# Performance work log

Hardware: AMD Instinct MI355X
Metric: run time of the kernel (lower is better)

The kernel has to match this reference:

```python
import jax, jax.numpy as jnp
import numpy as np

NUM_RELATIONS = 8
DROP_P = 0.2


def rgcn_layer(x, W, root, b, edge_index, edge_type, num_relations):
    # x: [N,F], W: [R,F,O], root: [F,O], b: [O]
    # edge_index: [2,E] (row 0 = source, row 1 = target), edge_type: [E]
    src, dst = edge_index[0], edge_index[1]
    N = x.shape[0]
    O = W.shape[2]
    # Transform all nodes under every relation once: [R,N,O]
    transformed = jnp.einsum('nf,rfo->rno', x, W)
    msg = transformed[edge_type, src]  # [E,O] gather per edge
    # mean aggregation per relation: per-(relation,target) in-degree
    deg = jnp.zeros((num_relations, N), x.dtype).at[edge_type, dst].add(1.0)
    coef = (1.0 / jnp.clip(deg, 1.0))[edge_type, dst]  # [E]
    agg = jnp.zeros((N, O), x.dtype).at[dst].add(msg * coef[:, None])
    return agg + x @ root + b


def setup_inputs() -> dict:
    key = jax.random.key(0)
    ks = jax.random.split(key, 10)
    N, E, F, H, O, R = 50000, 400000, 128, 128, 64, NUM_RELATIONS
    x = jax.random.normal(ks[0], (N, F), jnp.float32)
    edge_index = jax.random.randint(ks[1], (2, E), 0, N, jnp.int64)
    edge_type = jax.random.randint(ks[2], (E,), 0, R, jnp.int64)
    s = 1.0 / np.sqrt(F)
    W1 = jax.random.normal(ks[3], (R, F, H), jnp.float32) * s
    root1 = jax.random.normal(ks[4], (F, H), jnp.float32) * s
    b1 = jnp.zeros((H,), jnp.float32)
    sh = 1.0 / np.sqrt(H)
    W2 = jax.random.normal(ks[5], (R, H, O), jnp.float32) * sh
    root2 = jax.random.normal(ks[6], (H, O), jnp.float32) * sh
    b2 = jnp.zeros((O,), jnp.float32)
    # inverted dropout mask (training mode, p=0.2), precomputed for determinism
    keep = jax.random.bernoulli(ks[7], 1.0 - DROP_P, (N, H))
    drop_mask = keep.astype(jnp.float32) / (1.0 - DROP_P)
    return {"x": x, "edge_index": edge_index, "edge_type": edge_type,
            "W1": W1, "root1": root1, "b1": b1,
            "W2": W2, "root2": root2, "b2": b2, "drop_mask": drop_mask}


def reference(x, edge_index, edge_type, W1, root1, b1, W2, root2, b2, drop_mask):
    h = rgcn_layer(x, W1, root1, b1, edge_index, edge_type, NUM_RELATIONS)
    h = jax.nn.relu(h) * drop_mask  # fused relu + dropout
    out = rgcn_layer(h, W2, root2, b2, edge_index, edge_type, NUM_RELATIONS)
    return out
```

## Files before the change

### kernel.cpp

```cpp
#include <hip/hip_runtime.h>
#include <hip/hip_bf16.h>
#include <stdint.h>

typedef __attribute__((ext_vector_type(8))) short bf16x8;
typedef __attribute__((ext_vector_type(4))) float f32x4;

__device__ __forceinline__ unsigned f2bf(float f){
  unsigned u = __builtin_bit_cast(unsigned, f);
  return (u + 0x7FFFu + ((u >> 16) & 1u)) >> 16;
}
__device__ __forceinline__ float bf2f(unsigned s){
  unsigned u = s << 16; return __builtin_bit_cast(float, u);
}
__device__ __forceinline__ void add8(float* a, uint4 g){
  a[0] += bf2f(g.x & 0xFFFFu); a[1] += bf2f(g.x >> 16);
  a[2] += bf2f(g.y & 0xFFFFu); a[3] += bf2f(g.y >> 16);
  a[4] += bf2f(g.z & 0xFFFFu); a[5] += bf2f(g.z >> 16);
  a[6] += bf2f(g.w & 0xFFFFu); a[7] += bf2f(g.w >> 16);
}

__global__ void k_combo(const float* __restrict__ x,
                        const float* __restrict__ W1, const float* __restrict__ r1,
                        const float* __restrict__ W2, const float* __restrict__ r2,
                        const int* __restrict__ ei, const int* __restrict__ et,
                        short* __restrict__ Wt1, short* __restrict__ Wt2,
                        uint2* __restrict__ xb, int* __restrict__ degr,
                        int N, int E, int WB, int XB){
  int b = blockIdx.x, tid = threadIdx.x;
  if (b < WB){
    int t = b * 256 + tid;
    if (t < 128 * 1152){
      int o = t / 1152, ka = t - o * 1152, ph = ka >> 7, k = ka & 127;
      int kk = k >> 5, q = (k >> 3) & 3, j = k & 7;
      float v = (ph < 8) ? W1[(ph * 128 + k) * 128 + o] : r1[k * 128 + o];
      Wt1[(((ph * 4 + kk) * 4 + q) * 128 + o) * 8 + j] = (short)f2bf(v);
    } else if (t < 128 * 1152 + 64 * 1152){
      int t2 = t - 128 * 1152;
      int o = t2 / 1152, ka = t2 - o * 1152, ph = ka >> 7, k = ka & 127;
      int kk = k >> 5, q = (k >> 3) & 3, j = k & 7;
      float v = (ph < 8) ? W2[(ph * 128 + k) * 64 + o] : r2[k * 64 + o];
      Wt2[(((ph * 4 + kk) * 4 + q) * 64 + o) * 8 + j] = (short)f2bf(v);
    }
  } else if (b < WB + XB){
    int t = (b - WB) * 256 + tid;
    if (t < N * 32){
      float4 v = reinterpret_cast<const float4*>(x)[t];
      uint2 o;
      o.x = f2bf(v.x) | (f2bf(v.y) << 16);
      o.y = f2bf(v.z) | (f2bf(v.w) << 16);
      xb[t] = o;
    }
  } else {
    int e = (b - WB - XB) * 256 + tid;
    if (e < E){
      unsigned dst = (unsigned)ei[E + e];
      int rel = et[e] & 7;
      if (dst < (unsigned)N) atomicAdd(&degr[rel * N + dst], 1);
    }
  }
}

__global__ void k_scan(const int* __restrict__ cnt, int* __restrict__ gcnt,
                       int* __restrict__ offs, unsigned* __restrict__ pmeta, int M){
  __shared__ int s[256];
  __shared__ int sbase;
  int i = blockIdx.x * 256 + threadIdx.x;
  int v = (i < M) ? cnt[i] : 0;
  s[threadIdx.x] = v; __syncthreads();
  for (int d = 1; d < 256; d <<= 1){
    int t = (threadIdx.x >= d) ? s[threadIdx.x - d] : 0;
    __syncthreads();
    s[threadIdx.x] += t;
    __syncthreads();
  }
  if (threadIdx.x == 255) sbase = atomicAdd(gcnt, s[255]);
  __syncthreads();
  if (i < M){
    int off = sbase + s[threadIdx.x] - v;
    offs[i] = off;
    int c = v; if (c > 4095) c = 4095;
    pmeta[i] = (unsigned)off | ((unsigned)c << 20);
  }
}

__global__ void k_fill(const int* __restrict__ ei, const int* __restrict__ et,
                       const int* __restrict__ offs, int* __restrict__ fill,
                       unsigned short* __restrict__ idx, int E, int N){
  int e = blockIdx.x * 256 + threadIdx.x;
  if (e >= E) return;
  unsigned src = (unsigned)ei[e];
  unsigned dst = (unsigned)ei[E + e];
  int rel = et[e] & 7;
  if (dst < (unsigned)N){
    int key = rel * N + (int)dst;
    int p = atomicAdd(&fill[key], 1);
    idx[offs[key] + p] = (unsigned short)src;
  }
}

template<int NF, int MODE>
__global__ __launch_bounds__(256, 4)
void k_fused(const short* __restrict__ feat, const unsigned* __restrict__ pmeta,
             const unsigned short* __restrict__ idx2, const short* __restrict__ Wt,
             const float* __restrict__ bias, const float* __restrict__ mask,
             void* __restrict__ outp, int N){
  constexpr int BN = NF * 16;
  constexpr int NPW = NF / 4;
  __shared__ char sA[9 * 16 * 256];
  int tid = threadIdx.x, lane = tid & 63, wave = tid >> 6;
  int row0 = blockIdx.x * 16;

  {
    int r = tid >> 4, l = tid & 15;
    int dstj = row0 + r;
    bool vd = dstj < N;
    int dsafe = vd ? dstj : 0;
    unsigned m[8];
    #pragma unroll
    for (int ph = 0; ph < 8; ph++) m[ph] = vd ? pmeta[ph * N + dstj] : 0u;
    int s0[8], s1[8];
    #pragma unroll
    for (int ph = 0; ph < 8; ph++){
      int cnt = (int)(m[ph] >> 20), base = (int)(m[ph] & 0xFFFFFu);
      s0[ph] = (cnt > 0) ? (int)idx2[base] : 0;
      s1[ph] = (cnt > 1) ? (int)idx2[base + 1] : 0;
    }
    uint4 g0[8], g1[8], gr;
    #pragma unroll
    for (int ph = 0; ph < 8; ph++)
      g0[ph] = *reinterpret_cast<const uint4*>(feat + (size_t)s0[ph] * 128 + l * 8);
    #pragma unroll
    for (int ph = 0; ph < 8; ph++)
      g1[ph] = *reinterpret_cast<const uint4*>(feat + (size_t)s1[ph] * 128 + l * 8);
    gr = *reinterpret_cast<const uint4*>(feat + (size_t)dsafe * 128 + l * 8);

    int swz = (l ^ (r & 7)) << 4;
    #pragma unroll
    for (int ph = 0; ph < 8; ph++){
      int cnt = (int)(m[ph] >> 20), base = (int)(m[ph] & 0xFFFFFu);
      uint4 ov = {0u, 0u, 0u, 0u};
      if (cnt > 0){
        float a[8];
        a[0]=bf2f(g0[ph].x&0xFFFFu); a[1]=bf2f(g0[ph].x>>16);
        a[2]=bf2f(g0[ph].y&0xFFFFu); a[3]=bf2f(g0[ph].y>>16);
        a[4]=bf2f(g0[ph].z&0xFFFFu); a[5]=bf2f(g0[ph].z>>16);
        a[6]=bf2f(g0[ph].w&0xFFFFu); a[7]=bf2f(g0[ph].w>>16);
        if (cnt > 1) add8(a, g1[ph]);
        for (int i = 2; i < cnt; i++){
          int s = (int)idx2[base + i];
          uint4 gi = *reinterpret_cast<const uint4*>(feat + (size_t)s * 128 + l * 8);
          add8(a, gi);
        }
        float inv = 1.0f / (float)cnt;
        ov.x = f2bf(a[0]*inv) | (f2bf(a[1]*inv) << 16);
        ov.y = f2bf(a[2]*inv) | (f2bf(a[3]*inv) << 16);
        ov.z = f2bf(a[4]*inv) | (f2bf(a[5]*inv) << 16);
        ov.w = f2bf(a[6]*inv) | (f2bf(a[7]*inv) << 16);
      }
      *reinterpret_cast<uint4*>(sA + ph * 4096 + r * 256 + swz) = ov;
    }
    *reinterpret_cast<uint4*>(sA + 8 * 4096 + r * 256 + swz) = gr;
  }

  int r16 = lane & 15, q = lane >> 4;
  int obase = wave * NPW * 16 + r16;
  bf16x8 bb[2][4][NPW];
  #pragma unroll
  for (int kk = 0; kk < 4; kk++)
    #pragma unroll
    for (int nn = 0; nn < NPW; nn++)
      bb[0][kk][nn] = *reinterpret_cast<const bf16x8*>(
          Wt + ((size_t)(kk * 4 + q) * BN + obase + nn * 16) * 8);

  __syncthreads();

  f32x4 acc[NPW];
  f32x4 z = {0.f, 0.f, 0.f, 0.f};
  #pragma unroll
  for (int nn = 0; nn < NPW; nn++) acc[nn] = z;

  #pragma unroll
  for (int ph = 0; ph < 9; ph++){
    if (ph < 8){
      #pragma unroll
      for (int kk = 0; kk < 4; kk++)
        #pragma unroll
        for (int nn = 0; nn < NPW; nn++)
          bb[(ph + 1) & 1][kk][nn] = *reinterpret_cast<const bf16x8*>(
              Wt + ((size_t)(((ph + 1) * 4 + kk) * 4 + q) * BN + obase + nn * 16) * 8);
    }
    #pragma unroll
    for (int kk = 0; kk < 4; kk++){
      int ch = ((kk * 4 + q) ^ (r16 & 7)) << 4;
      bf16x8 av = *reinterpret_cast<const bf16x8*>(sA + ph * 4096 + r16 * 256 + ch);
      #pragma unroll
      for (int nn = 0; nn < NPW; nn++)
        acc[nn] = __builtin_amdgcn_mfma_f32_16x16x32_bf16(av, bb[ph & 1][kk][nn],
                                                          acc[nn], 0, 0, 0);
    }
  }

  #pragma unroll
  for (int nn = 0; nn < NPW; nn++){
    int col = obase + nn * 16;
    float bv = bias[col];
    #pragma unroll
    for (int j = 0; j < 4; j++){
      int row = row0 + (q << 2) + j;
      if (row < N){
        float v = acc[nn][j] + bv;
        if (MODE == 1){
          v = fmaxf(v, 0.f) * mask[(size_t)row * 128 + col];
          reinterpret_cast<short*>(outp)[(size_t)row * 128 + col] = (short)f2bf(v);
        } else {
          reinterpret_cast<float*>(outp)[(size_t)row * BN + col] = v;
        }
      }
    }
  }
}

extern "C" void kernel_launch(void* const* d_in, const int* in_sizes, int n_in,
                              void* d_out, int out_size, void* d_ws, size_t ws_size,
                              hipStream_t stream){
  const float* x    = (const float*)d_in[0];
  const int*   ei   = (const int*)d_in[1];
  const int*   et   = (const int*)d_in[2];
  const float* W1   = (const float*)d_in[3];
  const float* r1   = (const float*)d_in[4];
  const float* b1   = (const float*)d_in[5];
  const float* W2   = (const float*)d_in[6];
  const float* r2   = (const float*)d_in[7];
  const float* b2   = (const float*)d_in[8];
  const float* mask = (const float*)d_in[9];
  int N = in_sizes[0] / 128;
  int E = in_sizes[2];
  int M8 = 8 * N;

  char* ws = (char*)d_ws;
  short*    xb    = (short*)(ws + 0);
  short*    hb    = (short*)(ws + 12800000);
  short*    Wt1   = (short*)(ws + 25600000);
  short*    Wt2   = (short*)(ws + 25894912);
  int*      degr  = (int*)(ws + 26042368);
  int*      fill  = (int*)(ws + 27642368);
  int*      gcnt  = (int*)(ws + 29242368);
  int*      offs2 = (int*)(ws + 29242432);
  unsigned* pmeta = (unsigned*)(ws + 30842432);
  unsigned short* idx2 = (unsigned short*)(ws + 32442432);
  if (ws_size < (size_t)32442432 + (size_t)E * 2 + 64) return;

  hipMemsetAsync(degr, 0, (size_t)M8 * 8 + 64, stream);

  int WB = (128*1152 + 64*1152 + 255) / 256;
  int XB = (N * 32 + 255) / 256;
  int EB = (E + 255) / 256;
  int NB = (M8 + 255) / 256;
  k_combo<<<WB + XB + EB, 256, 0, stream>>>(x, W1, r1, W2, r2, ei, et,
                                            Wt1, Wt2, (uint2*)xb, degr, N, E, WB, XB);
  k_scan<<<NB, 256, 0, stream>>>(degr, gcnt, offs2, pmeta, M8);
  k_fill<<<EB, 256, 0, stream>>>(ei, et, offs2, fill, idx2, E, N);

  int G = (N + 15) / 16;
  k_fused<8, 1><<<G, 256, 0, stream>>>(xb, pmeta, idx2, Wt1, b1, mask, hb, N);
  k_fused<4, 2><<<G, 256, 0, stream>>>(hb, pmeta, idx2, Wt2, b2, nullptr, d_out, N);
}
```

Before: 281.3 us.

## Stage first gathered neighbor rows directly into LDS and stream weights per MFMA

The first neighbor row per relation is now loaded with global_load_lds straight into shared memory, with zero-padded sentinel rows so empty relations need no branching. Nodes with more than one neighbor accumulate and rewrite their LDS slot. The self-row is held in registers instead of a ninth LDS phase. Weight fragments are read from global memory right before each MFMA instead of being double-buffered in registers, which cuts register pressure but exposes load latency. The workspace layout gains padding so the sentinel rows can be zeroed.

After: 284.6 us. No clear change (+1.2%).

```diff
diff --git a/kernel.cpp b/kernel.cpp
--- a/kernel.cpp
+++ b/kernel.cpp
@@ -17,6 +17,10 @@
   a[2] += bf2f(g.y & 0xFFFFu); a[3] += bf2f(g.y >> 16);
   a[4] += bf2f(g.z & 0xFFFFu); a[5] += bf2f(g.z >> 16);
   a[6] += bf2f(g.w & 0xFFFFu); a[7] += bf2f(g.w >> 16);
+}
+__device__ __forceinline__ void stage16(const void* g, void* l){
+  __builtin_amdgcn_global_load_lds((const __attribute__((address_space(1))) void*)g,
+                                   (__attribute__((address_space(3))) void*)l, 16, 0, 0);
 }
 
 __global__ void k_combo(const float* __restrict__ x,
@@ -106,97 +110,96 @@
              void* __restrict__ outp, int N){
   constexpr int BN = NF * 16;
   constexpr int NPW = NF / 4;
-  __shared__ char sA[9 * 16 * 256];
+  __shared__ char sA[8 * 16 * 256];
   int tid = threadIdx.x, lane = tid & 63, wave = tid >> 6;
   int row0 = blockIdx.x * 16;
-
-  {
-    int r = tid >> 4, l = tid & 15;
-    int dstj = row0 + r;
-    bool vd = dstj < N;
-    int dsafe = vd ? dstj : 0;
-    unsigned m[8];
-    #pragma unroll
-    for (int ph = 0; ph < 8; ph++) m[ph] = vd ? pmeta[ph * N + dstj] : 0u;
-    int s0[8], s1[8];
-    #pragma unroll
-    for (int ph = 0; ph < 8; ph++){
-      int cnt = (int)(m[ph] >> 20), base = (int)(m[ph] & 0xFFFFFu);
-      s0[ph] = (cnt > 0) ? (int)idx2[base] : 0;
-      s1[ph] = (cnt > 1) ? (int)idx2[base + 1] : 0;
-    }
-    uint4 g0[8], g1[8], gr;
-    #pragma unroll
-    for (int ph = 0; ph < 8; ph++)
-      g0[ph] = *reinterpret_cast<const uint4*>(feat + (size_t)s0[ph] * 128 + l * 8);
-    #pragma unroll
-    for (int ph = 0; ph < 8; ph++)
-      g1[ph] = *reinterpret_cast<const uint4*>(feat + (size_t)s1[ph] * 128 + l * 8);
-    gr = *reinterpret_cast<const uint4*>(feat + (size_t)dsafe * 128 + l * 8);
-
-    int swz = (l ^ (r & 7)) << 4;
-    #pragma unroll
-    for (int ph = 0; ph < 8; ph++){
-      int cnt = (int)(m[ph] >> 20), base = (int)(m[ph] & 0xFFFFFu);
-      uint4 ov = {0u, 0u, 0u, 0u};
-      if (cnt > 0){
-        float a[8];
-        a[0]=bf2f(g0[ph].x&0xFFFFu); a[1]=bf2f(g0[ph].x>>16);
-        a[2]=bf2f(g0[ph].y&0xFFFFu); a[3]=bf2f(g0[ph].y>>16);
-        a[4]=bf2f(g0[ph].z&0xFFFFu); a[5]=bf2f(g0[ph].z>>16);
-        a[6]=bf2f(g0[ph].w&0xFFFFu); a[7]=bf2f(g0[ph].w>>16);
-        if (cnt > 1) add8(a, g1[ph]);
-        for (int i = 2; i < cnt; i++){
-          int s = (int)idx2[base + i];
-          uint4 gi = *reinterpret_cast<const uint4*>(feat + (size_t)s * 128 + l * 8);
-          add8(a, gi);
-        }
-        float inv = 1.0f / (float)cnt;
-        ov.x = f2bf(a[0]*inv) | (f2bf(a[1]*inv) << 16);
-        ov.y = f2bf(a[2]*inv) | (f2bf(a[3]*inv) << 16);
-        ov.z = f2bf(a[4]*inv) | (f2bf(a[5]*inv) << 16);
-        ov.w = f2bf(a[6]*inv) | (f2bf(a[7]*inv) << 16);
-      }
-      *reinterpret_cast<uint4*>(sA + ph * 4096 + r * 256 + swz) = ov;
-    }
-    *reinterpret_cast<uint4*>(sA + 8 * 4096 + r * 256 + swz) = gr;
+  int r = tid >> 4, l = tid & 15;
+  int dstj = row0 + r;
+  bool vd = dstj < N;
+  int c = l ^ (r & 7);
+
+  unsigned m[8];
+  #pragma unroll
+  for (int ph = 0; ph < 8; ph++) m[ph] = vd ? pmeta[ph * N + dstj] : 0u;
+  int s0[8];
+  #pragma unroll
+  for (int ph = 0; ph < 8; ph++){
+    int cnt = (int)(m[ph] >> 20), base = (int)(m[ph] & 0xFFFFFu);
+    s0[ph] = (cnt > 0) ? (int)idx2[base] : N;
+  }
+  #pragma unroll
+  for (int ph = 0; ph < 8; ph++)
+    stage16(feat + (size_t)s0[ph] * 128 + c * 8, sA + ph * 4096 + wave * 1024);
+
+  uint4 g1[8];
+  #pragma unroll
+  for (int ph = 0; ph < 8; ph++){
+    int cnt = (int)(m[ph] >> 20), base = (int)(m[ph] & 0xFFFFFu);
+    if (cnt > 1)
+      g1[ph] = *reinterpret_cast<const uint4*>(
+          feat + (size_t)(int)idx2[base + 1] * 128 + c * 8);
   }
 
   int r16 = lane & 15, q = lane >> 4;
-  int obase = wave * NPW * 16 + r16;
-  bf16x8 bb[2][4][NPW];
+  int rsafe = row0 + r16; if (rsafe > N) rsafe = N;
+  bf16x8 avr[4];
   #pragma unroll
   for (int kk = 0; kk < 4; kk++)
-    #pragma unroll
-    for (int nn = 0; nn < NPW; nn++)
-      bb[0][kk][nn] = *reinterpret_cast<const bf16x8*>(
-          Wt + ((size_t)(kk * 4 + q) * BN + obase + nn * 16) * 8);
-
+    avr[kk] = *reinterpret_cast<const bf16x8*>(
+        feat + (size_t)rsafe * 128 + kk * 32 + q * 8);
+
+  asm volatile("s_waitcnt vmcnt(0)" ::: "memory");
+
+  #pragma unroll
+  for (int ph = 0; ph < 8; ph++){
+    int cnt = (int)(m[ph] >> 20), base = (int)(m[ph] & 0xFFFFFu);
+    if (cnt > 1){
+      uint4 v = *reinterpret_cast<uint4*>(sA + ph * 4096 + r * 256 + l * 16);
+      float a[8];
+      a[0]=bf2f(v.x&0xFFFFu); a[1]=bf2f(v.x>>16);
+      a[2]=bf2f(v.y&0xFFFFu); a[3]=bf2f(v.y>>16);
+      a[4]=bf2f(v.z&0xFFFFu); a[5]=bf2f(v.z>>16);
+      a[6]=bf2f(v.w&0xFFFFu); a[7]=bf2f(v.w>>16);
+      add8(a, g1[ph]);
+      for (int i = 2; i < cnt; i++){
+        int s = (int)idx2[base + i];
+        uint4 gi = *reinterpret_cast<const uint4*>(feat + (size_t)s * 128 + c * 8);
+        add8(a, gi);
+      }
+      float inv = 1.0f / (float)cnt;
+      uint4 o;
+      o.x = f2bf(a[0]*inv) | (f2bf(a[1]*inv) << 16);
+      o.y = f2bf(a[2]*inv) | (f2bf(a[3]*inv) << 16);
+      o.z = f2bf(a[4]*inv) | (f2bf(a[5]*inv) << 16);
+      o.w = f2bf(a[6]*inv) | (f2bf(a[7]*inv) << 16);
+      *reinterpret_cast<uint4*>(sA + ph * 4096 + r * 256 + l * 16) = o;
+    }
+  }
   __syncthreads();
 
   f32x4 acc[NPW];
   f32x4 z = {0.f, 0.f, 0.f, 0.f};
   #pragma unroll
   for (int nn = 0; nn < NPW; nn++) acc[nn] = z;
+  int obase = wave * NPW * 16 + r16;
 
   #pragma unroll
   for (int ph = 0; ph < 9; ph++){
-    if (ph < 8){
-      #pragma unroll
-      for (int kk = 0; kk < 4; kk++)
-        #pragma unroll
-        for (int nn = 0; nn < NPW; nn++)
-          bb[(ph + 1) & 1][kk][nn] = *reinterpret_cast<const bf16x8*>(
-              Wt + ((size_t)(((ph + 1) * 4 + kk) * 4 + q) * BN + obase + nn * 16) * 8);
-    }
     #pragma unroll
     for (int kk = 0; kk < 4; kk++){
-      int ch = ((kk * 4 + q) ^ (r16 & 7)) << 4;
-      bf16x8 av = *reinterpret_cast<const bf16x8*>(sA + ph * 4096 + r16 * 256 + ch);
+      bf16x8 av;
+      if (ph < 8){
+        int ch = ((kk * 4 + q) ^ (r16 & 7)) << 4;
+        av = *reinterpret_cast<const bf16x8*>(sA + ph * 4096 + r16 * 256 + ch);
+      } else {
+        av = avr[kk];
+      }
       #pragma unroll
-      for (int nn = 0; nn < NPW; nn++)
-        acc[nn] = __builtin_amdgcn_mfma_f32_16x16x32_bf16(av, bb[ph & 1][kk][nn],
-                                                          acc[nn], 0, 0, 0);
+      for (int nn = 0; nn < NPW; nn++){
+        bf16x8 bv = *reinterpret_cast<const bf16x8*>(
+            Wt + ((size_t)((ph * 4 + kk) * 4 + q) * BN + obase + nn * 16) * 8);
+        acc[nn] = __builtin_amdgcn_mfma_f32_16x16x32_bf16(av, bv, acc[nn], 0, 0, 0);
+      }
     }
   }
 
@@ -239,18 +242,20 @@
 
   char* ws = (char*)d_ws;
   short*    xb    = (short*)(ws + 0);
-  short*    hb    = (short*)(ws + 12800000);
-  short*    Wt1   = (short*)(ws + 25600000);
-  short*    Wt2   = (short*)(ws + 25894912);
-  int*      degr  = (int*)(ws + 26042368);
-  int*      fill  = (int*)(ws + 27642368);
-  int*      gcnt  = (int*)(ws + 29242368);
-  int*      offs2 = (int*)(ws + 29242432);
-  unsigned* pmeta = (unsigned*)(ws + 30842432);
-  unsigned short* idx2 = (unsigned short*)(ws + 32442432);
-  if (ws_size < (size_t)32442432 + (size_t)E * 2 + 64) return;
+  short*    hb    = (short*)(ws + 12800512);
+  short*    Wt1   = (short*)(ws + 25601024);
+  short*    Wt2   = (short*)(ws + 25895936);
+  int*      degr  = (int*)(ws + 26043392);
+  int*      fill  = (int*)(ws + 27643392);
+  int*      gcnt  = (int*)(ws + 29243392);
+  int*      offs2 = (int*)(ws + 29243456);
+  unsigned* pmeta = (unsigned*)(ws + 30843456);
+  unsigned short* idx2 = (unsigned short*)(ws + 32443456);
+  if (ws_size < (size_t)32443456 + (size_t)E * 2 + 64) return;
 
   hipMemsetAsync(degr, 0, (size_t)M8 * 8 + 64, stream);
+  hipMemsetAsync(xb + (size_t)N * 128, 0, 256, stream);
+  hipMemsetAsync(hb + (size_t)N * 128, 0, 256, stream);
 
   int WB = (128*1152 + 64*1152 + 255) / 256;
   int XB = (N * 32 + 255) / 256;
```
